# Optimization experiments

Hardware: AMD Instinct MI355X
Metric: run time of the kernel (lower is better)

Reference implementation:

```python
import jax, jax.numpy as jnp
import numpy as np

N_NODES = 100000
N_EDGES = 1600000
IN_DIM = 64
HID_DIM = 64
NUM_CLASSES = 10
NUM_GRAPHS = 64


def setup_inputs() -> dict:
    key = jax.random.key(0)
    ks = jax.random.split(key, 8)
    x = jax.random.normal(ks[0], (N_NODES, IN_DIM), dtype=jnp.float32)
    edge_index = jax.random.randint(ks[1], (2, N_EDGES), 0, N_NODES, dtype=jnp.int32)
    batch = jnp.sort(jax.random.randint(ks[2], (N_NODES,), 0, NUM_GRAPHS, dtype=jnp.int32))
    # GCNConv weights (glorot-ish scale) and biases
    W1 = jax.random.normal(ks[3], (IN_DIM, HID_DIM), dtype=jnp.float32) / np.sqrt(IN_DIM)
    b1 = jnp.zeros((HID_DIM,), dtype=jnp.float32)
    W2 = jax.random.normal(ks[4], (HID_DIM, HID_DIM), dtype=jnp.float32) / np.sqrt(HID_DIM)
    b2 = jnp.zeros((HID_DIM,), dtype=jnp.float32)
    Wlin = jax.random.normal(ks[5], (HID_DIM, NUM_CLASSES), dtype=jnp.float32) / np.sqrt(HID_DIM)
    blin = jnp.zeros((NUM_CLASSES,), dtype=jnp.float32)
    return {"x": x, "edge_index": edge_index, "batch": batch,
            "W1": W1, "b1": b1, "W2": W2, "b2": b2, "Wlin": Wlin, "blin": blin}


def _gcn_conv(h, src, dst, norm, W, b, n_nodes):
    # h' = scatter_add( norm * (h W)[src] -> dst ) + b   (symmetric-normalized A+I)
    m = (h @ W)[src] * norm[:, None]          # [E+N, hid] edge messages (incl. self-loops)
    out = jax.ops.segment_sum(m, dst, num_segments=n_nodes)
    return out + b


def reference(x, edge_index, batch, W1, b1, W2, b2, Wlin, blin):
    n = x.shape[0]
    loops = jnp.arange(n, dtype=edge_index.dtype)
    src = jnp.concatenate([edge_index[0], loops])  # A + I self-loops
    dst = jnp.concatenate([edge_index[1], loops])
    deg = jax.ops.segment_sum(jnp.ones_like(dst, dtype=x.dtype), dst, num_segments=n)
    dinv = jax.lax.rsqrt(jnp.maximum(deg, 1.0))
    norm = dinv[src] * dinv[dst]               # D^{-1/2} (A+I) D^{-1/2} edge weights

    h = jax.nn.relu(_gcn_conv(x, src, dst, norm, W1, b1, n))
    h = jax.nn.relu(_gcn_conv(h, src, dst, norm, W2, b2, n))

    # global_mean_pool over batch segments
    sums = jax.ops.segment_sum(h, batch, num_segments=NUM_GRAPHS)
    cnts = jax.ops.segment_sum(jnp.ones((n,), dtype=h.dtype), batch, num_segments=NUM_GRAPHS)
    pooled = sums / jnp.maximum(cnts, 1.0)[:, None]
    return pooled @ Wlin + blin                # [G, num_classes]
```

## Files before the change

### kernel.cpp

```cpp
#include <hip/hip_runtime.h>
#include <hip/hip_bf16.h>


#define NDIM 64
#define NGRAPH 64
#define NREP 32
#define BSHIFT 7
#define BNODES 128
#define PADSLOT (BNODES * 16)
#define ECHUNK 2048
#define EPB (ECHUNK / 256)

#define BLO(u) __uint_as_float((u) << 16)
#define BHI(u) __uint_as_float((u) & 0xFFFF0000u)

__device__ __forceinline__ unsigned short f32_to_bf16(float f) {
    unsigned int u = __float_as_uint(f);
    unsigned int r = 0x7FFFu + ((u >> 16) & 1u);
    return (unsigned short)((u + r) >> 16);
}

__global__ void bincnt_k(const int* __restrict__ dst, int* __restrict__ cntmat,
                         int e, int nb) {
    extern __shared__ int hist[];
    int t = threadIdx.x;
    for (int i = t; i < nb; i += 256) hist[i] = 0;
    __syncthreads();
    int base = blockIdx.x * ECHUNK + t;
#pragma unroll
    for (int k = 0; k < EPB; ++k) {
        int i = base + k * 256;
        if (i < e) atomicAdd(&hist[dst[i] >> BSHIFT], 1);
    }
    __syncthreads();
    long row = (long)blockIdx.x * nb;
    for (int i = t; i < nb; i += 256) cntmat[row + i] = hist[i];
}

__global__ void colscan_k(const int* __restrict__ cntmat, int* __restrict__ basemat,
                          int* __restrict__ bucketTot, float* __restrict__ pooledR,
                          int nblk, int nb) {
    __shared__ int s[1024];
    int b = blockIdx.x;
    int t = threadIdx.x;
    int z = b * 1024 + t;
    if (z < NREP * NGRAPH * NDIM) pooledR[z] = 0.f;
    int v = (t < nblk) ? cntmat[(long)t * nb + b] : 0;
    s[t] = v;
    __syncthreads();
    for (int off = 1; off < 1024; off <<= 1) {
        int tmp = (t >= off) ? s[t - off] : 0;
        __syncthreads();
        s[t] += tmp;
        __syncthreads();
    }
    if (t < nblk) basemat[(long)t * nb + b] = s[t] - v;
    if (t == 1023) bucketTot[b] = s[1023];
}

__global__ void bscan_k(const int* __restrict__ bucketTot, int* __restrict__ bucketStart,
                        int* __restrict__ start, int* __restrict__ gstart,
                        int* __restrict__ gend, int nb, int n, int e) {
    __shared__ int s[1024];
    int t = threadIdx.x;
    if (t < NGRAPH) { gstart[t] = 0; gend[t] = 0; }
    int v = (t < nb) ? bucketTot[t] : 0;
    s[t] = v;
    __syncthreads();
    for (int off = 1; off < 1024; off <<= 1) {
        int tmp = (t >= off) ? s[t - off] : 0;
        __syncthreads();
        s[t] += tmp;
        __syncthreads();
    }
    if (t < nb) bucketStart[t + 1] = s[t];
    if (t == 0) { bucketStart[0] = 0; start[n] = e; }
}

__global__ void bscatter_k(const int* __restrict__ src, const int* __restrict__ dst,
                           const int* __restrict__ bucketStart,
                           const int* __restrict__ basemat,
                           unsigned int* __restrict__ ebuf, int e, int nb) {
    extern __shared__ int cur[];
    int t = threadIdx.x;
    long row = (long)blockIdx.x * nb;
    for (int i = t; i < nb; i += 256) cur[i] = bucketStart[i] + basemat[row + i];
    __syncthreads();
    int base = blockIdx.x * ECHUNK + t;
#pragma unroll
    for (int k = 0; k < EPB; ++k) {
        int i = base + k * 256;
        if (i < e) {
            int d = dst[i];
            int b = d >> BSHIFT;
            int pos = atomicAdd(&cur[b], 1);
            ebuf[pos] = ((unsigned)(d & (BNODES - 1)) << 25) | (unsigned)src[i];
        }
    }
}

__global__ void fill2_k(const unsigned int* __restrict__ ebuf,
                        const int* __restrict__ bucketStart,
                        const int* __restrict__ batch, float* __restrict__ dinv,
                        int* __restrict__ start, int* __restrict__ m16,
                        int* __restrict__ csr,
                        int* __restrict__ gstart, int* __restrict__ gend, int n) {
    __shared__ int scnt[BNODES], sincl[BNODES], scur[BNODES];
    int t = threadIdx.x;
    int b = blockIdx.x;
    int node0 = b << BSHIFT;
    int nNodes = min(BNODES, n - node0);
    if (t < BNODES) scnt[t] = 0;
    int e0 = bucketStart[b], e1 = bucketStart[b + 1];
    __syncthreads();
    for (int i = e0 + t; i < e1; i += 256)
        atomicAdd(&scnt[ebuf[i] >> 25], 1);
    __syncthreads();
    int val = (t < BNODES) ? scnt[t] : 0;
    int slots = (t < nNodes) ? ((val + 16) & ~15) : 0;
    if (t < BNODES) sincl[t] = slots;
    __syncthreads();
    for (int off = 1; off < BNODES; off <<= 1) {
        int tmp = (t >= off && t < BNODES) ? sincl[t - off] : 0;
        __syncthreads();
        if (t < BNODES) sincl[t] += tmp;
        __syncthreads();
    }
    if (t < nNodes) {
        int v = node0 + t;
        int st = e0 + b * PADSLOT + sincl[t] - slots;
        start[v] = st;
        m16[v] = slots >> 4;
        scur[t] = st;
        dinv[v] = rsqrtf((float)(val + 1));
        csr[st + val] = v;
        for (int k2 = val + 1; k2 < slots; ++k2) csr[st + k2] = n;
        int g = batch[v];
        if (v == 0 || batch[v - 1] != g) gstart[g] = v;
        if (v == n - 1 || batch[v + 1] != g) gend[g] = v + 1;
    }
    __syncthreads();
    for (int i = e0 + t; i < e1; i += 256) {
        unsigned rec = ebuf[i];
        int pos = atomicAdd(&scur[rec >> 25], 1);
        csr[pos] = (int)(rec & 0x1FFFFFFu);
    }
}

__global__ void gemm_k(const float* __restrict__ A, const float* __restrict__ W,
                       const float* __restrict__ scale,
                       unsigned long long* __restrict__ C, int n) {
    __shared__ float4 Wl4[64 * 16];
    __shared__ float4 Xl4[64 * 16];
    int t = threadIdx.x;
    if (blockIdx.x == 0 && t < 16) C[(long)n * 16 + t] = 0ULL;
    const float4* W4 = (const float4*)W;
#pragma unroll
    for (int i = 0; i < 4; ++i) Wl4[t + 256 * i] = W4[t + 256 * i];
    const float4* A4 = (const float4*)A;
    long fbase = (long)blockIdx.x * 1024;
    long fmax  = (long)n * 16;
#pragma unroll
    for (int i = 0; i < 4; ++i) {
        long f = fbase + t + 256 * i;
        float4 v;
        if (f < fmax) v = A4[f];
        else { v.x = 0.f; v.y = 0.f; v.z = 0.f; v.w = 0.f; }
        Xl4[t + 256 * i] = v;
    }
    __syncthreads();
    int rg = t >> 4, cg = t & 15;
    float a00 = 0.f, a01 = 0.f, a02 = 0.f, a03 = 0.f;
    float a10 = 0.f, a11 = 0.f, a12 = 0.f, a13 = 0.f;
    float a20 = 0.f, a21 = 0.f, a22 = 0.f, a23 = 0.f;
    float a30 = 0.f, a31 = 0.f, a32 = 0.f, a33 = 0.f;
#pragma unroll 4
    for (int k4 = 0; k4 < 16; ++k4) {
        float4 w0 = Wl4[(4 * k4 + 0) * 16 + cg];
        float4 w1 = Wl4[(4 * k4 + 1) * 16 + cg];
        float4 w2 = Wl4[(4 * k4 + 2) * 16 + cg];
        float4 w3 = Wl4[(4 * k4 + 3) * 16 + cg];
        float4 x0 = Xl4[(4 * rg + 0) * 16 + k4];
        float4 x1 = Xl4[(4 * rg + 1) * 16 + k4];
        float4 x2 = Xl4[(4 * rg + 2) * 16 + k4];
        float4 x3 = Xl4[(4 * rg + 3) * 16 + k4];
        a00 += x0.x * w0.x + x0.y * w1.x + x0.z * w2.x + x0.w * w3.x;
        a01 += x0.x * w0.y + x0.y * w1.y + x0.z * w2.y + x0.w * w3.y;
        a02 += x0.x * w0.z + x0.y * w1.z + x0.z * w2.z + x0.w * w3.z;
        a03 += x0.x * w0.w + x0.y * w1.w + x0.z * w2.w + x0.w * w3.w;
        a10 += x1.x * w0.x + x1.y * w1.x + x1.z * w2.x + x1.w * w3.x;
        a11 += x1.x * w0.y + x1.y * w1.y + x1.z * w2.y + x1.w * w3.y;
        a12 += x1.x * w0.z + x1.y * w1.z + x1.z * w2.z + x1.w * w3.z;
        a13 += x1.x * w0.w + x1.y * w1.w + x1.z * w2.w + x1.w * w3.w;
        a20 += x2.x * w0.x + x2.y * w1.x + x2.z * w2.x + x2.w * w3.x;
        a21 += x2.x * w0.y + x2.y * w1.y + x2.z * w2.y + x2.w * w3.y;
        a22 += x2.x * w0.z + x2.y * w1.z + x2.z * w2.z + x2.w * w3.z;
        a23 += x2.x * w0.w + x2.y * w1.w + x2.z * w2.w + x2.w * w3.w;
        a30 += x3.x * w0.x + x3.y * w1.x + x3.z * w2.x + x3.w * w3.x;
        a31 += x3.x * w0.y + x3.y * w1.y + x3.z * w2.y + x3.w * w3.y;
        a32 += x3.x * w0.z + x3.y * w1.z + x3.z * w2.z + x3.w * w3.z;
        a33 += x3.x * w0.w + x3.y * w1.w + x3.z * w2.w + x3.w * w3.w;
    }
    int vb = blockIdx.x * 64 + rg * 4;
    int v;
    float s;
    unsigned long long u;
    v = vb + 0;
    if (v < n) {
        s = scale[v];
        u  = (unsigned long long)(((unsigned int)f32_to_bf16(s * a01) << 16) | (unsigned int)f32_to_bf16(s * a00));
        u |= (unsigned long long)(((unsigned int)f32_to_bf16(s * a03) << 16) | (unsigned int)f32_to_bf16(s * a02)) << 32;
        C[(long)v * 16 + cg] = u;
    }
    v = vb + 1;
    if (v < n) {
        s = scale[v];
        u  = (unsigned long long)(((unsigned int)f32_to_bf16(s * a11) << 16) | (unsigned int)f32_to_bf16(s * a10));
        u |= (unsigned long long)(((unsigned int)f32_to_bf16(s * a13) << 16) | (unsigned int)f32_to_bf16(s * a12)) << 32;
        C[(long)v * 16 + cg] = u;
    }
    v = vb + 2;
    if (v < n) {
        s = scale[v];
        u  = (unsigned long long)(((unsigned int)f32_to_bf16(s * a21) << 16) | (unsigned int)f32_to_bf16(s * a20));
        u |= (unsigned long long)(((unsigned int)f32_to_bf16(s * a23) << 16) | (unsigned int)f32_to_bf16(s * a22)) << 32;
        C[(long)v * 16 + cg] = u;
    }
    v = vb + 3;
    if (v < n) {
        s = scale[v];
        u  = (unsigned long long)(((unsigned int)f32_to_bf16(s * a31) << 16) | (unsigned int)f32_to_bf16(s * a30));
        u |= (unsigned long long)(((unsigned int)f32_to_bf16(s * a33) << 16) | (unsigned int)f32_to_bf16(s * a32)) << 32;
        C[(long)v * 16 + cg] = u;
    }
}

template <class F>
__device__ __forceinline__ void gather_stream(const unsigned int* __restrict__ xp,
                                              const int* __restrict__ csr,
                                              int c0, int m0, int m1, int m2, int m3,
                                              int nv, int h, int p, F fin) {
    int M = m0;
    if (nv > 1) M += m1;
    if (nv > 2) M += m2;
    if (nv > 3) M += m3;
    int c = c0 + h;
    int j0 = csr[c +  0];
    int j1 = csr[c +  2];
    int j2 = csr[c +  4];
    int j3 = csr[c +  6];
    int j4 = csr[c +  8];
    int j5 = csr[c + 10];
    int j6 = csr[c + 12];
    int j7 = csr[c + 14];
    float l0 = 0.f, l1 = 0.f, l2 = 0.f, l3 = 0.f;
    float h0 = 0.f, h1 = 0.f, h2 = 0.f, h3 = 0.f;
    int mrem = m0, cur = 0;
    for (int it = 0; it < M; ++it) {
        unsigned int u0 = xp[(long)j0 * 32 + p];
        unsigned int u1 = xp[(long)j1 * 32 + p];
        unsigned int u2 = xp[(long)j2 * 32 + p];
        unsigned int u3 = xp[(long)j3 * 32 + p];
        unsigned int u4 = xp[(long)j4 * 32 + p];
        unsigned int u5 = xp[(long)j5 * 32 + p];
        unsigned int u6 = xp[(long)j6 * 32 + p];
        unsigned int u7 = xp[(long)j7 * 32 + p];
        c += 16;
        int t0 = csr[c +  0];
        int t1 = csr[c +  2];
        int t2 = csr[c +  4];
        int t3 = csr[c +  6];
        int t4 = csr[c +  8];
        int t5 = csr[c + 10];
        int t6 = csr[c + 12];
        int t7 = csr[c + 14];
        l0 += BLO(u0);  h0 += BHI(u0);
        l1 += BLO(u1);  h1 += BHI(u1);
        l2 += BLO(u2);  h2 += BHI(u2);
        l3 += BLO(u3);  h3 += BHI(u3);
        l0 += BLO(u4);  h0 += BHI(u4);
        l1 += BLO(u5);  h1 += BHI(u5);
        l2 += BLO(u6);  h2 += BHI(u6);
        l3 += BLO(u7);  h3 += BHI(u7);
        j0 = t0; j1 = t1; j2 = t2; j3 = t3;
        j4 = t4; j5 = t5; j6 = t6; j7 = t7;
        if (--mrem == 0) {
            float al = (l0 + l1) + (l2 + l3);
            float ah = (h0 + h1) + (h2 + h3);
            al += __shfl_xor(al, 32);
            ah += __shfl_xor(ah, 32);
            fin(cur, h ? ah : al);
            l0 = l1 = l2 = l3 = 0.f;
            h0 = h1 = h2 = h3 = 0.f;
            ++cur;
            mrem = (cur == 1) ? m1 : ((cur == 2) ? m2 : m3);
        }
    }
}

__global__ void agg_k(const unsigned int* __restrict__ xp, const float* __restrict__ dinv,
                      const int* __restrict__ start, const int* __restrict__ m16,
                      const int* __restrict__ csr, const float* __restrict__ bias,
                      float* __restrict__ out, int n) {
    int t = threadIdx.x;
    int lane = t & 63;
    int h = lane >> 5;
    int p = lane & 31;
    int wid = blockIdx.x * 4 + (t >> 6);
    int v0 = wid * 4;
    if (v0 >= n) return;
    int nv = min(4, n - v0);
    int4 ss = *(const int4*)&start[v0];
    int4 mm = *(const int4*)&m16[v0];
    float4 dv = *(const float4*)&dinv[v0];
    int d = 2 * p + h;
    float b = bias[d];
    float* orow = out + (long)v0 * NDIM + d;
    gather_stream(xp, csr, ss.x, mm.x, mm.y, mm.z, mm.w, nv, h, p,
        [&](int cur, float sum) {
            float dvv = (cur == 0) ? dv.x : (cur == 1) ? dv.y : (cur == 2) ? dv.z : dv.w;
            orow[(long)cur * NDIM] = fmaxf(fmaf(sum, dvv, b), 0.f);
        });
}

__global__ void aggpool_k(const unsigned int* __restrict__ xp, const float* __restrict__ dinv,
                          const int* __restrict__ start, const int* __restrict__ m16,
                          const int* __restrict__ csr, const float* __restrict__ b2,
                          const int* __restrict__ batch, float* __restrict__ pooledR, int n) {
    int t = threadIdx.x;
    int lane = t & 63;
    int h = lane >> 5, p = lane & 31;
    int wid = blockIdx.x * 4 + (t >> 6);
    int v0 = wid * 4;
    if (v0 >= n) return;
    int nv = min(4, n - v0);
    int4 ss = *(const int4*)&start[v0];
    int4 mm = *(const int4*)&m16[v0];
    float4 dv = *(const float4*)&dinv[v0];
    int4 bt = *(const int4*)&batch[v0];
    int d = 2 * p + h;
    float bias = b2[d];
    long rbase = (long)(wid & (NREP - 1)) * (NGRAPH * NDIM);
    int gcur = -1;
    float acc = 0.f;
    gather_stream(xp, csr, ss.x, mm.x, mm.y, mm.z, mm.w, nv, h, p,
        [&](int cur, float sum) {
            int g = (cur == 0) ? bt.x : (cur == 1) ? bt.y : (cur == 2) ? bt.z : bt.w;
            float dvv = (cur == 0) ? dv.x : (cur == 1) ? dv.y : (cur == 2) ? dv.z : dv.w;
            if (g != gcur) {
                if (gcur >= 0) atomicAdd(&pooledR[rbase + gcur * NDIM + d], acc);
                gcur = g;
                acc = 0.f;
            }
            acc += fmaxf(fmaf(sum, dvv, bias), 0.f);
        });
    if (gcur >= 0) atomicAdd(&pooledR[rbase + gcur * NDIM + d], acc);
}

__global__ void reduce_k(const float* __restrict__ pooledR, float* __restrict__ pooled) {
    int t = blockIdx.x * 256 + threadIdx.x;
    if (t >= NGRAPH * NDIM) return;
    float s = 0.f;
#pragma unroll
    for (int r = 0; r < NREP; ++r) s += pooledR[(long)r * (NGRAPH * NDIM) + t];
    pooled[t] = s;
}

__global__ void final_k(const float* __restrict__ pooled, const int* __restrict__ gstart,
                        const int* __restrict__ gend,
                        const float* __restrict__ Wlin, const float* __restrict__ blin,
                        float* __restrict__ out, int nclass) {
    int t = blockIdx.x * blockDim.x + threadIdx.x;
    if (t >= NGRAPH * nclass) return;
    int g = t / nclass, c = t % nclass;
    float cnt = (float)(gend[g] - gstart[g]);
    float inv = 1.f / fmaxf(cnt, 1.f);
    float acc = 0.f;
    for (int j = 0; j < NDIM; ++j) acc += pooled[g * NDIM + j] * Wlin[j * nclass + c];
    out[t] = acc * inv + blin[c];
}

extern "C" void kernel_launch(void* const* d_in, const int* in_sizes, int n_in,
                              void* d_out, int out_size, void* d_ws, size_t ws_size,
                              hipStream_t stream) {
    const float* x     = (const float*)d_in[0];
    const int*   ei    = (const int*)d_in[1];
    const int*   batch = (const int*)d_in[2];
    const float* W1    = (const float*)d_in[3];
    const float* b1    = (const float*)d_in[4];
    const float* W2    = (const float*)d_in[5];
    const float* b2    = (const float*)d_in[6];
    const float* Wlin  = (const float*)d_in[7];
    const float* blin  = (const float*)d_in[8];
    float* out = (float*)d_out;

    const int N = in_sizes[0] / NDIM;
    const int E = in_sizes[1] / 2;
    const int NCLASS = in_sizes[7] / NDIM;
    const int* src = ei;
    const int* dst = ei + E;
    const int NB   = (N + BNODES - 1) >> BSHIFT;
    const int NBLK = (E + ECHUNK - 1) / ECHUNK;

    size_t o = 0;
    char* wsp = (char*)d_ws;
    auto take = [&](size_t nbytes) -> void* {
        void* p = (void*)(wsp + o);
        o += (nbytes + 255) & ~(size_t)255;
        return p;
    };
    int*   gstart    = (int*)take(NGRAPH * 4);
    int*   gend      = (int*)take(NGRAPH * 4);
    float* pooledR   = (float*)take((size_t)NREP * NGRAPH * NDIM * 4);
    float* pooled    = (float*)take(NGRAPH * NDIM * 4);
    int*   cntmat   = (int*)take((size_t)NBLK * NB * 4);
    int*   basemat  = (int*)take((size_t)NBLK * NB * 4);
    int*   bucketTot   = (int*)take((size_t)NB * 4);
    int*   bucketStart = (int*)take((size_t)(NB + 1) * 4);
    float* dinv  = (float*)take((size_t)N * 4);
    int*   start = (int*)take((size_t)(N + 1) * 4);
    int*   m16   = (int*)take((size_t)N * 4);
    int*   csr   = (int*)take(((size_t)E + (size_t)NB * PADSLOT + 64) * 4);
    unsigned int* xws  = (unsigned int*)take((size_t)(N + 1) * NDIM * 2);
    float* h     = (float*)take((size_t)N * NDIM * 4);
    unsigned int* ebuf = (unsigned int*)h;
    (void)ws_size;

    int rbl = (N + 15) / 16;
    int gbl = (N + 63) / 64;

    bincnt_k<<<NBLK, 256, (size_t)NB * 4, stream>>>(dst, cntmat, E, NB);
    colscan_k<<<NB, 1024, 0, stream>>>(cntmat, basemat, bucketTot, pooledR, NBLK, NB);
    bscan_k<<<1, 1024, 0, stream>>>(bucketTot, bucketStart, start, gstart, gend, NB, N, E);
    bscatter_k<<<NBLK, 256, (size_t)NB * 4, stream>>>(src, dst, bucketStart, basemat, ebuf, E, NB);
    fill2_k<<<NB, 256, 0, stream>>>(ebuf, bucketStart, batch, dinv, start, m16, csr, gstart, gend, N);

    gemm_k<<<gbl, 256, 0, stream>>>(x, W1, dinv, (unsigned long long*)xws, N);
    agg_k<<<rbl, 256, 0, stream>>>(xws, dinv, start, m16, csr, b1, h, N);
    gemm_k<<<gbl, 256, 0, stream>>>(h, W2, dinv, (unsigned long long*)xws, N);
    aggpool_k<<<rbl, 256, 0, stream>>>(xws, dinv, start, m16, csr, b2, batch, pooledR, N);
    reduce_k<<<(NGRAPH * NDIM + 255) / 256, 256, 0, stream>>>(pooledR, pooled);
    final_k<<<(NGRAPH * NCLASS + 255) / 256, 256, 0, stream>>>(pooled, gstart, gend, Wlin, blin, out, NCLASS);
}
```

Baseline: 250.8 us.

## Fuse layer-1 aggregation with layer-2 linear transform in one kernel

Replaces the separate aggregation and second GEMM with a single kernel. Each 1024-thread block gathers 64 nodes into shared memory, applies bias and ReLU, then multiplies by W2 and writes bf16 scaled output. This removes the fp32 hidden-feature write and re-read plus one launch. In exchange it uses large blocks with a sync between the gather and GEMM phases, which may reduce occupancy, and it adds a second bf16 buffer.

```diff
diff --git a/kernel.cpp b/kernel.cpp
--- a/kernel.cpp
+++ b/kernel.cpp
@@ -298,29 +298,57 @@
     }
 }
 
-__global__ void agg_k(const unsigned int* __restrict__ xp, const float* __restrict__ dinv,
-                      const int* __restrict__ start, const int* __restrict__ m16,
-                      const int* __restrict__ csr, const float* __restrict__ bias,
-                      float* __restrict__ out, int n) {
-    int t = threadIdx.x;
-    int lane = t & 63;
-    int h = lane >> 5;
-    int p = lane & 31;
-    int wid = blockIdx.x * 4 + (t >> 6);
-    int v0 = wid * 4;
-    if (v0 >= n) return;
-    int nv = min(4, n - v0);
-    int4 ss = *(const int4*)&start[v0];
-    int4 mm = *(const int4*)&m16[v0];
-    float4 dv = *(const float4*)&dinv[v0];
-    int d = 2 * p + h;
-    float b = bias[d];
-    float* orow = out + (long)v0 * NDIM + d;
-    gather_stream(xp, csr, ss.x, mm.x, mm.y, mm.z, mm.w, nv, h, p,
-        [&](int cur, float sum) {
-            float dvv = (cur == 0) ? dv.x : (cur == 1) ? dv.y : (cur == 2) ? dv.z : dv.w;
-            orow[(long)cur * NDIM] = fmaxf(fmaf(sum, dvv, b), 0.f);
-        });
+__global__ __launch_bounds__(1024) void agglin_k(
+        const unsigned int* __restrict__ xp, const float* __restrict__ dinv,
+        const int* __restrict__ start, const int* __restrict__ m16,
+        const int* __restrict__ csr, const float* __restrict__ b1,
+        const float* __restrict__ W2, unsigned long long* __restrict__ C, int n) {
+    __shared__ float4 Wl4[64 * 16];
+    __shared__ float4 Hl4[64 * 17];
+    int t = threadIdx.x;
+    Wl4[t] = ((const float4*)W2)[t];
+    if (blockIdx.x == 0 && t < 16) C[(long)n * 16 + t] = 0ULL;
+    int node0 = blockIdx.x * 64;
+    int w = t >> 6, lane = t & 63;
+    int h = lane >> 5, p = lane & 31;
+    int v0 = node0 + w * 4;
+    float* Hs = (float*)Hl4;
+    if (v0 < n) {
+        int nv = min(4, n - v0);
+        int4 ss = *(const int4*)&start[v0];
+        int4 mm = *(const int4*)&m16[v0];
+        float4 dv = *(const float4*)&dinv[v0];
+        int d = 2 * p + h;
+        float b = b1[d];
+        float* hrow = Hs + (w * 4) * 68 + d;
+        gather_stream(xp, csr, ss.x, mm.x, mm.y, mm.z, mm.w, nv, h, p,
+            [&](int cur, float sum) {
+                float dvv = (cur == 0) ? dv.x : (cur == 1) ? dv.y : (cur == 2) ? dv.z : dv.w;
+                hrow[cur * 68] = fmaxf(fmaf(sum, dvv, b), 0.f);
+            });
+    }
+    __syncthreads();
+    int rg = t >> 4, cg = t & 15;
+    int v = node0 + rg;
+    if (v >= n) return;
+    float a0 = 0.f, a1 = 0.f, a2 = 0.f, a3 = 0.f;
+#pragma unroll 4
+    for (int k4 = 0; k4 < 16; ++k4) {
+        float4 w0 = Wl4[(4 * k4 + 0) * 16 + cg];
+        float4 w1 = Wl4[(4 * k4 + 1) * 16 + cg];
+        float4 w2 = Wl4[(4 * k4 + 2) * 16 + cg];
+        float4 w3 = Wl4[(4 * k4 + 3) * 16 + cg];
+        float4 x  = Hl4[rg * 17 + k4];
+        a0 += x.x * w0.x + x.y * w1.x + x.z * w2.x + x.w * w3.x;
+        a1 += x.x * w0.y + x.y * w1.y + x.z * w2.y + x.w * w3.y;
+        a2 += x.x * w0.z + x.y * w1.z + x.z * w2.z + x.w * w3.z;
+        a3 += x.x * w0.w + x.y * w1.w + x.z * w2.w + x.w * w3.w;
+    }
+    float s = dinv[v];
+    unsigned long long u;
+    u  = (unsigned long long)(((unsigned int)f32_to_bf16(s * a1) << 16) | (unsigned int)f32_to_bf16(s * a0));
+    u |= (unsigned long long)(((unsigned int)f32_to_bf16(s * a3) << 16) | (unsigned int)f32_to_bf16(s * a2)) << 32;
+    C[(long)v * 16 + cg] = u;
 }
 
 __global__ void aggpool_k(const unsigned int* __restrict__ xp, const float* __restrict__ dinv,
@@ -420,10 +448,10 @@
     float* dinv  = (float*)take((size_t)N * 4);
     int*   start = (int*)take((size_t)(N + 1) * 4);
     int*   m16   = (int*)take((size_t)N * 4);
-    int*   csr   = (int*)take(((size_t)E + (size_t)NB * PADSLOT + 64) * 4);
-    unsigned int* xws  = (unsigned int*)take((size_t)(N + 1) * NDIM * 2);
-    float* h     = (float*)take((size_t)N * NDIM * 4);
-    unsigned int* ebuf = (unsigned int*)h;
+    int*   csr   = (int*)take(((size_t)E + (size_t)NB * PADSLOT + 256) * 4);
+    unsigned int* xws   = (unsigned int*)take((size_t)(N + 1) * NDIM * 2);
+    unsigned int* xws2  = (unsigned int*)take((size_t)(N + 1) * NDIM * 2);
+    unsigned int* ebuf  = (unsigned int*)take((size_t)E * 4);
     (void)ws_size;
 
     int rbl = (N + 15) / 16;
@@ -436,9 +464,9 @@
     fill2_k<<<NB, 256, 0, stream>>>(ebuf, bucketStart, batch, dinv, start, m16, csr, gstart, gend, N);
 
     gemm_k<<<gbl, 256, 0, stream>>>(x, W1, dinv, (unsigned long long*)xws, N);
-    agg_k<<<rbl, 256, 0, stream>>>(xws, dinv, start, m16, csr, b1, h, N);
-    gemm_k<<<gbl, 256, 0, stream>>>(h, W2, dinv, (unsigned long long*)xws, N);
-    aggpool_k<<<rbl, 256, 0, stream>>>(xws, dinv, start, m16, csr, b2, batch, pooledR, N);
+    agglin_k<<<gbl, 1024, 0, stream>>>(xws, dinv, start, m16, csr, b1, W2,
+                                       (unsigned long long*)xws2, N);
+    aggpool_k<<<rbl, 256, 0, stream>>>(xws2, dinv, start, m16, csr, b2, batch, pooledR, N);
     reduce_k<<<(NGRAPH * NDIM + 255) / 256, 256, 0, stream>>>(pooledR, pooled);
     final_k<<<(NGRAPH * NCLASS + 255) / 256, 256, 0, stream>>>(pooled, gstart, gend, Wlin, blin, out, NCLASS);
 }
```

After: 247.7 us. About the same (-1.2%).
